# Optimization experiments

Measured on AMD Instinct MI355X. Metric: run time of the kernel, lower is better.

## Reference

```python
import jax, jax.numpy as jnp
import numpy as np


def setup_inputs() -> dict:
    key = jax.random.key(0)
    k1, k2, k3, k4 = jax.random.split(key, 4)
    B, H, W, C, NCLS = 128, 14, 14, 512, 200
    # post-ReLU-like non-negative feature map
    x = jax.random.uniform(k1, (B, H, W, C), dtype=jnp.float32)
    # one-hot-like logits for ground-truth labels (only argmax is used)
    gt = jax.random.normal(k2, (B, NCLS), dtype=jnp.float32)
    # positional template codebook; index [H, W] (== shape[0]-1) is the sentinel
    # 'negative' template used for all-zero channels
    t_p = jax.random.normal(k3, (H + 1, W + 1, H, W), dtype=jnp.float32)
    # per-class channel template, broadcast-multiplied with masked features
    class_templates = jax.random.uniform(k4, (NCLS, H, W, C), dtype=jnp.float32)
    return {"x": x, "gt": gt, "t_p": t_p, "class_templates": class_templates}


def reference(x, gt, t_p, class_templates):
    # x: [B, H, W, C] channels-last feature map
    B, H, W, C = x.shape
    flat = x.reshape(B, H * W, C)
    # global spatial argmax per (batch, channel) == max_pool_with_argmax over full extent
    idx = jnp.argmax(flat, axis=1)            # [B, C]
    h = idx // W                               # [B, C]
    w = idx % W                                # [B, C]
    # channels whose spatial max is exactly 0 get the sentinel template index
    empty = jnp.max(flat, axis=1) == 0.0       # [B, C]
    sentinel = t_p.shape[0] - 1
    h = jnp.where(empty, sentinel, h)
    w = jnp.where(empty, sentinel, w)
    # gather positional templates: [B, C, H, W] -> [B, H, W, C]
    templates = jnp.transpose(t_p[h, w], (0, 2, 3, 1))
    masked = jax.nn.relu(x * templates)
    # training branch with gt, reduce_loss=False: mask by the class template
    cls = jnp.argmax(gt, axis=1)               # [B]
    masked = masked * class_templates[cls]     # [B, H, W, C]
    return (masked, x, templates)
```

## Files before the change

kernel.cpp:

```cpp
#include <hip/hip_runtime.h>

#define B    128
#define H    14
#define W    14
#define C    512
#define NCLS 200
#define HW   (H * W)
#define TP_DIM 15
#define SENT_OFF ((14 * TP_DIM + 14) * HW)

typedef float  v4f __attribute__((ext_vector_type(4)));
typedef int    v4i __attribute__((ext_vector_type(4)));

__global__ __launch_bounds__(256) void argmax_kernel(
        const float* __restrict__ x,
        const float* __restrict__ gt,
        int* __restrict__ hwoff,
        int* __restrict__ cls) {
    int idx = blockIdx.x * 256 + threadIdx.x;
    int b = idx >> 9;
    int c = idx & (C - 1);

    const float* xp = x + (size_t)b * HW * C + c;
    float best = xp[0];
    int bi = 0;
#pragma unroll 14
    for (int s = 1; s < HW; ++s) {
        float v = xp[(size_t)s * C];
        if (v > best) { best = v; bi = s; }
    }
    int off;
    if (best == 0.0f) {
        off = SENT_OFF;
    } else {
        int h = bi / W;
        int w = bi - h * W;
        off = (h * TP_DIM + w) * HW;
    }
    hwoff[idx] = off;

    if (idx < B) {
        const float* g = gt + (size_t)idx * NCLS;
        float gb = g[0];
        int gi = 0;
        for (int i = 1; i < NCLS; ++i) {
            float v = g[i];
            if (v > gb) { gb = v; gi = i; }
        }
        cls[idx] = gi;
    }
}

__global__ __launch_bounds__(128) void main_kernel(
        const float* __restrict__ x,
        const float* __restrict__ t_p,
        const float* __restrict__ ctpl,
        const int*   __restrict__ hwoff,
        const int*   __restrict__ cls,
        float*       __restrict__ out) {
    int blk = blockIdx.x;
    int b   = blk / 49;
    int s0  = (blk - b * 49) * 4;
    int c0  = threadIdx.x * 4;

    v4i off = *(const v4i*)(hwoff + b * C + c0);
    int klass = cls[b];

    v4f t0 = *(const v4f*)(t_p + off.x + s0);
    v4f t1 = *(const v4f*)(t_p + off.y + s0);
    v4f t2 = *(const v4f*)(t_p + off.z + s0);
    v4f t3 = *(const v4f*)(t_p + off.w + s0);
    v4f tv[4];
    tv[0] = (v4f){t0.x, t1.x, t2.x, t3.x};
    tv[1] = (v4f){t0.y, t1.y, t2.y, t3.y};
    tv[2] = (v4f){t0.z, t1.z, t2.z, t3.z};
    tv[3] = (v4f){t0.w, t1.w, t2.w, t3.w};

    const size_t plane = (size_t)B * HW * C;
    const size_t base  = ((size_t)b * HW + s0) * C + c0;
    const float* __restrict__ xp = x + base;
    const float* __restrict__ cp = ctpl + ((size_t)klass * HW + s0) * C + c0;
    float* __restrict__ out_m = out + base;
    float* __restrict__ out_x = out + plane + base;
    float* __restrict__ out_t = out + 2 * plane + base;

#pragma unroll
    for (int i = 0; i < 4; ++i) {
        v4f xv = *(const v4f*)(xp + (size_t)i * C);
        v4f ct = *(const v4f*)(cp + (size_t)i * C);
        v4f t  = tv[i];
        v4f m;
        m.x = fmaxf(xv.x * t.x, 0.0f) * ct.x;
        m.y = fmaxf(xv.y * t.y, 0.0f) * ct.y;
        m.z = fmaxf(xv.z * t.z, 0.0f) * ct.z;
        m.w = fmaxf(xv.w * t.w, 0.0f) * ct.w;
        __builtin_nontemporal_store(m,  (v4f*)(out_m + (size_t)i * C));
        __builtin_nontemporal_store(xv, (v4f*)(out_x + (size_t)i * C));
        __builtin_nontemporal_store(t,  (v4f*)(out_t + (size_t)i * C));
    }
}

extern "C" void kernel_launch(void* const* d_in, const int* in_sizes, int n_in,
                              void* d_out, int out_size, void* d_ws, size_t ws_size,
                              hipStream_t stream) {
    const float* x    = (const float*)d_in[0];
    const float* gt   = (const float*)d_in[1];
    const float* t_p  = (const float*)d_in[2];
    const float* ctpl = (const float*)d_in[3];
    float* out = (float*)d_out;

    int* hwoff = (int*)d_ws;
    int* cls   = hwoff + (size_t)B * C;

    hipLaunchKernelGGL(argmax_kernel,
                       dim3((B * C) / 256), dim3(256), 0, stream,
                       x, gt, hwoff, cls);

    hipLaunchKernelGGL(main_kernel,
                       dim3(B * (HW / 4)), dim3(128), 0, stream,
                       x, t_p, ctpl, hwoff, cls, out);
}
```

Baseline: 280.6 us.

## Fuse argmax and masking into one kernel with per-batch shared offsets

Merges the argmax pass and the elementwise masking pass into one kernel launched with two blocks per batch. Each block recomputes the per-channel spatial argmax into shared memory and computes the class argmax with a wavefront shuffle reduction. The block then processes its half of the spatial quads. This drops a launch and the workspace round trip, but both blocks of a batch read x twice for the argmax, and the grid shrinks to 256 large blocks, which may leave fewer waves in flight to hide latency.

```diff
diff --git a/kernel.cpp b/kernel.cpp
--- a/kernel.cpp
+++ b/kernel.cpp
@@ -12,91 +12,107 @@
 typedef float  v4f __attribute__((ext_vector_type(4)));
 typedef int    v4i __attribute__((ext_vector_type(4)));
 
-__global__ __launch_bounds__(256) void argmax_kernel(
+__global__ __launch_bounds__(512) void fused_kernel(
         const float* __restrict__ x,
         const float* __restrict__ gt,
-        int* __restrict__ hwoff,
-        int* __restrict__ cls) {
-    int idx = blockIdx.x * 256 + threadIdx.x;
-    int b = idx >> 9;
-    int c = idx & (C - 1);
+        const float* __restrict__ t_p,
+        const float* __restrict__ ctpl,
+        float*       __restrict__ out) {
+    __shared__ int s_off[C];
+    __shared__ int s_cls;
 
-    const float* xp = x + (size_t)b * HW * C + c;
-    float best = xp[0];
-    int bi = 0;
-#pragma unroll 14
-    for (int s = 1; s < HW; ++s) {
-        float v = xp[(size_t)s * C];
-        if (v > best) { best = v; bi = s; }
+    const int tid  = threadIdx.x;
+    const int b    = blockIdx.x >> 1;
+    const int half = blockIdx.x & 1;
+
+    {
+        const float* xp = x + (size_t)b * HW * C + tid;
+        float best = xp[0];
+        int   bs   = 0;
+#pragma unroll 13
+        for (int s = 1; s < HW; ++s) {
+            float v = xp[(size_t)s * C];
+            if (v > best) { best = v; bs = s; }
+        }
+        int off;
+        if (best == 0.0f) {
+            off = SENT_OFF;
+        } else {
+            int h = bs / W;
+            int w = bs - h * W;
+            off = (h * TP_DIM + w) * HW;
+        }
+        s_off[tid] = off;
     }
-    int off;
-    if (best == 0.0f) {
-        off = SENT_OFF;
-    } else {
-        int h = bi / W;
-        int w = bi - h * W;
-        off = (h * TP_DIM + w) * HW;
-    }
-    hwoff[idx] = off;
 
-    if (idx < B) {
-        const float* g = gt + (size_t)idx * NCLS;
-        float gb = g[0];
-        int gi = 0;
-        for (int i = 1; i < NCLS; ++i) {
+    if (tid < 64) {
+        const float* g = gt + (size_t)b * NCLS;
+        float gb = -__builtin_inff();
+        int   gi = NCLS;
+        for (int i = tid; i < NCLS; i += 64) {
             float v = g[i];
             if (v > gb) { gb = v; gi = i; }
         }
-        cls[idx] = gi;
+#pragma unroll
+        for (int d = 1; d < 64; d <<= 1) {
+            float ov = __shfl_xor(gb, d);
+            int   oi = __shfl_xor(gi, d);
+            if (ov > gb || (ov == gb && oi < gi)) { gb = ov; gi = oi; }
+        }
+        if (tid == 0) s_cls = gi;
     }
-}
 
-__global__ __launch_bounds__(128) void main_kernel(
-        const float* __restrict__ x,
-        const float* __restrict__ t_p,
-        const float* __restrict__ ctpl,
-        const int*   __restrict__ hwoff,
-        const int*   __restrict__ cls,
-        float*       __restrict__ out) {
-    int blk = blockIdx.x;
-    int b   = blk / 49;
-    int s0  = (blk - b * 49) * 4;
-    int c0  = threadIdx.x * 4;
+    __syncthreads();
 
-    v4i off = *(const v4i*)(hwoff + b * C + c0);
-    int klass = cls[b];
-
-    v4f t0 = *(const v4f*)(t_p + off.x + s0);
-    v4f t1 = *(const v4f*)(t_p + off.y + s0);
-    v4f t2 = *(const v4f*)(t_p + off.z + s0);
-    v4f t3 = *(const v4f*)(t_p + off.w + s0);
-    v4f tv[4];
-    tv[0] = (v4f){t0.x, t1.x, t2.x, t3.x};
-    tv[1] = (v4f){t0.y, t1.y, t2.y, t3.y};
-    tv[2] = (v4f){t0.z, t1.z, t2.z, t3.z};
-    tv[3] = (v4f){t0.w, t1.w, t2.w, t3.w};
+    const int klass   = s_cls;
+    const int q_base  = half ? 25 : 0;
+    const int n_quads = half ? 24 : 25;
+    const int n_tiles = n_quads * 128;
 
     const size_t plane = (size_t)B * HW * C;
-    const size_t base  = ((size_t)b * HW + s0) * C + c0;
-    const float* __restrict__ xp = x + base;
-    const float* __restrict__ cp = ctpl + ((size_t)klass * HW + s0) * C + c0;
-    float* __restrict__ out_m = out + base;
-    float* __restrict__ out_x = out + plane + base;
-    float* __restrict__ out_t = out + 2 * plane + base;
+
+    for (int e = tid; e < n_tiles; e += 512) {
+        int cg = e & 127;
+        int q  = e >> 7;
+        int s0 = (q_base + q) * 4;
+        int c0 = cg * 4;
+
+        int o0 = s_off[c0 + 0];
+        int o1 = s_off[c0 + 1];
+        int o2 = s_off[c0 + 2];
+        int o3 = s_off[c0 + 3];
+
+        v4f t0 = *(const v4f*)(t_p + o0 + s0);
+        v4f t1 = *(const v4f*)(t_p + o1 + s0);
+        v4f t2 = *(const v4f*)(t_p + o2 + s0);
+        v4f t3 = *(const v4f*)(t_p + o3 + s0);
+        v4f tv[4];
+        tv[0] = (v4f){t0.x, t1.x, t2.x, t3.x};
+        tv[1] = (v4f){t0.y, t1.y, t2.y, t3.y};
+        tv[2] = (v4f){t0.z, t1.z, t2.z, t3.z};
+        tv[3] = (v4f){t0.w, t1.w, t2.w, t3.w};
+
+        const size_t base = ((size_t)b * HW + s0) * C + c0;
+        const float* __restrict__ xp = x + base;
+        const float* __restrict__ cp = ctpl + ((size_t)klass * HW + s0) * C + c0;
+        float* __restrict__ out_m = out + base;
+        float* __restrict__ out_x = out + plane + base;
+        float* __restrict__ out_t = out + 2 * plane + base;
 
 #pragma unroll
-    for (int i = 0; i < 4; ++i) {
-        v4f xv = *(const v4f*)(xp + (size_t)i * C);
-        v4f ct = *(const v4f*)(cp + (size_t)i * C);
-        v4f t  = tv[i];
-        v4f m;
-        m.x = fmaxf(xv.x * t.x, 0.0f) * ct.x;
-        m.y = fmaxf(xv.y * t.y, 0.0f) * ct.y;
-        m.z = fmaxf(xv.z * t.z, 0.0f) * ct.z;
-        m.w = fmaxf(xv.w * t.w, 0.0f) * ct.w;
-        __builtin_nontemporal_store(m,  (v4f*)(out_m + (size_t)i * C));
-        __builtin_nontemporal_store(xv, (v4f*)(out_x + (size_t)i * C));
-        __builtin_nontemporal_store(t,  (v4f*)(out_t + (size_t)i * C));
+        for (int i = 0; i < 4; ++i) {
+            v4f xv = *(const v4f*)(xp + (size_t)i * C);
+            v4f ct = *(const v4f*)(cp + (size_t)i * C);
+            v4f t  = tv[i];
+            v4f m;
+            m.x = fmaxf(xv.x * t.x, 0.0f) * ct.x;
+            m.y = fmaxf(xv.y * t.y, 0.0f) * ct.y;
+            m.z = fmaxf(xv.z * t.z, 0.0f) * ct.z;
+            m.w = fmaxf(xv.w * t.w, 0.0f) * ct.w;
+            __builtin_nontemporal_store(m,  (v4f*)(out_m + (size_t)i * C));
+            __builtin_nontemporal_store(xv, (v4f*)(out_x + (size_t)i * C));
+            __builtin_nontemporal_store(t,  (v4f*)(out_t + (size_t)i * C));
+        }
     }
 }
 
@@ -109,14 +125,7 @@
     const float* ctpl = (const float*)d_in[3];
     float* out = (float*)d_out;
 
-    int* hwoff = (int*)d_ws;
-    int* cls   = hwoff + (size_t)B * C;
-
-    hipLaunchKernelGGL(argmax_kernel,
-                       dim3((B * C) / 256), dim3(256), 0, stream,
-                       x, gt, hwoff, cls);
-
-    hipLaunchKernelGGL(main_kernel,
-                       dim3(B * (HW / 4)), dim3(128), 0, stream,
-                       x, t_p, ctpl, hwoff, cls, out);
+    hipLaunchKernelGGL(fused_kernel,
+                       dim3(2 * B), dim3(512), 0, stream,
+                       x, gt, t_p, ctpl, out);
 }
```

Measured after the change: 266.6 us. 1.05x faster.
